# Optimization experiments

Hardware: AMD Instinct MI355X
Metric: run time of the kernel (lower is better)

Reference implementation:

```python
import jax, jax.numpy as jnp
import numpy as np

N_NODE = 100000
H = 128          # hidden_size
N_INTEREST = 4
B = 4096         # batch
T = 50           # session length


def setup_inputs() -> dict:
    key = jax.random.key(0)
    ks = jax.random.split(key, 8)
    stdv = 1.0 / np.sqrt(H)
    u = lambda k, s: jax.random.uniform(k, s, jnp.float32, -stdv, stdv)
    return {
        "inputs": jax.random.randint(ks[0], (B, T), 0, N_NODE),
        "embedding": u(ks[1], (N_NODE, H)),            # nn.Embedding weight
        "w_interest": u(ks[2], (N_INTEREST, H)),       # Linear(H -> n_interest, bias=False)
        "w_ih": u(ks[3], (N_INTEREST, 3 * H, H)),      # per-interest GNN params
        "w_hh": u(ks[4], (N_INTEREST, 3 * H, H)),
        "b_ih": u(ks[5], (N_INTEREST, 3 * H)),
        "b_hh": u(ks[6], (N_INTEREST, 3 * H)),
        "h0": jax.random.normal(ks[7], (N_INTEREST, B, H), jnp.float32),  # torch.randn init state
    }


def _gru_interest(w_ih, w_hh, b_ih, b_hh, h0, g_t, x_t):
    """Custom gated recurrence for one interest. x_t: [T,B,H], g_t: [T,B]."""
    def step(h, inp):
        x, gv = inp
        gi = x @ w_ih.T + b_ih          # [B, 3H]
        gh = h @ w_hh.T + b_hh          # [B, 3H]
        i_r, i_i, i_n = jnp.split(gi, 3, axis=1)
        h_r, h_i, h_n = jnp.split(gh, 3, axis=1)
        resetgate = jax.nn.sigmoid(i_r + h_r)
        inputgate = jax.nn.sigmoid(i_i + h_i)
        newgate = jnp.tanh(i_n + resetgate * h_n)
        g = gv[:, None]                  # [B, 1]
        concentrgate = jnp.where(g > 0.01, 1.0, 0.0) * g * inputgate
        hy = (1.0 - concentrgate) * h + concentrgate * newgate
        return hy, None
    h_last, _ = jax.lax.scan(step, h0, (x_t, g_t))
    return h_last                        # [B, H]


def reference(inputs, embedding, w_interest, w_ih, w_hh, b_ih, b_hh, h0):
    hidden = embedding[inputs]                                   # [B, T, H]
    # item_weight_for_interest: softmax over interests with temperature 0.1
    g = jax.nn.softmax((hidden @ w_interest.T) / 0.1, axis=2)    # [B, T, I]
    x_t = jnp.transpose(hidden, (1, 0, 2))                       # [T, B, H]
    g_t = jnp.transpose(g, (2, 1, 0))                            # [I, T, B]
    out = jax.vmap(_gru_interest, in_axes=(0, 0, 0, 0, 0, 0, None))(
        w_ih, w_hh, b_ih, b_hh, h0, g_t, x_t)                    # [I, B, H]
    return jnp.transpose(out, (1, 0, 2))                         # [B, I, H]
```

## Files before the change

kernel.cpp:

```cpp
#include <hip/hip_runtime.h>
#include <hip/hip_bf16.h>

#define NB 4096
#define NT 50
#define NH 128
#define NINT 4
#define ROWS 64

typedef float f32x4 __attribute__((ext_vector_type(4)));
typedef __bf16 bf16x8 __attribute__((ext_vector_type(8)));
typedef short short8 __attribute__((ext_vector_type(8)));
typedef short short4s __attribute__((ext_vector_type(4)));

#define L2E 1.4426950408889634f

__device__ __forceinline__ float frcp(float x) { return __builtin_amdgcn_rcpf(x); }

__device__ __forceinline__ float exp2neg(float x) {
  float r;
  asm("v_exp_f32 %0, -%1" : "=v"(r) : "v"(x));
  return r;
}

__device__ __forceinline__ unsigned short bfbits(float f) {
  __bf16 b = (__bf16)f;
  return __builtin_bit_cast(unsigned short, b);
}

__global__ __launch_bounds__(512, 2)
void gru_fused(const int* __restrict__ inputs, const float* __restrict__ emb,
               const float* __restrict__ w_int, const float* __restrict__ w_ih,
               const float* __restrict__ w_hh, const float* __restrict__ b_ih,
               const float* __restrict__ b_hh, const float* __restrict__ h0,
               float* __restrict__ out) {
  __shared__ unsigned short xs[2][ROWS * NH];
  __shared__ unsigned short hs[2][ROWS * NH];
  __shared__ int idxs[NT * ROWS];

  const int tid = threadIdx.x;
  const int bx = blockIdx.x;
  const int I = bx >> 6;
  const int R0 = (bx & 63) * ROWS;
  const int w = tid >> 6;
  const int lane = tid & 63;
  const int l15 = lane & 15;
  const int l4 = lane >> 4;
  const int oc0 = w * 16 + l4 * 4;

  const int sr = tid >> 3;
  const int sp = tid & 7;

  for (int e = tid; e < NT * ROWS; e += 512) {
    int t = e >> 6, r = e & (ROWS - 1);
    idxs[e] = inputs[(size_t)(R0 + r) * NT + t];
  }
  __syncthreads();

  bf16x8 wih[3][4], whh[3][4];
  f32x4 bR, bI, bNI, bNH;
  {
    const float gs[3] = {L2E, L2E, 2.0f * L2E};
    #pragma unroll
    for (int g = 0; g < 3; ++g) {
      int oc = g * NH + w * 16 + l15;
      #pragma unroll
      for (int kk = 0; kk < 4; ++kk) {
        int k0 = kk * 32 + l4 * 8;
        const float* pi = w_ih + ((size_t)(I * 384 + oc) * NH + k0);
        const float* ph = w_hh + ((size_t)(I * 384 + oc) * NH + k0);
        bf16x8 si, sh;
        #pragma unroll
        for (int e = 0; e < 8; ++e) {
          si[e] = (__bf16)(pi[e] * gs[g]);
          sh[e] = (__bf16)(ph[e] * gs[g]);
        }
        wih[g][kk] = si;
        whh[g][kk] = sh;
      }
    }
    #pragma unroll
    for (int j = 0; j < 4; ++j) {
      bR[j] = (b_ih[I * 384 + oc0 + j] + b_hh[I * 384 + oc0 + j]) * L2E;
      bI[j] = (b_ih[I * 384 + NH + oc0 + j] + b_hh[I * 384 + NH + oc0 + j]) * L2E;
      bNI[j] = b_ih[I * 384 + 2 * NH + oc0 + j] * (2.0f * L2E);
      bNH[j] = b_hh[I * 384 + 2 * NH + oc0 + j] * (2.0f * L2E);
    }
  }

  bf16x8 wg[4];
  #pragma unroll
  for (int kk = 0; kk < 4; ++kk) {
    bf16x8 f;
    #pragma unroll
    for (int e = 0; e < 8; ++e) {
      float v = (l15 < NINT)
                    ? w_int[l15 * NH + kk * 32 + l4 * 8 + e] * (10.0f * L2E)
                    : 0.0f;
      f[e] = (__bf16)v;
    }
    wg[kk] = f;
  }

  float hm[4][4];
  #pragma unroll
  for (int m = 0; m < 4; ++m) {
    int row = m * 16 + l15;
    short4s p;
    #pragma unroll
    for (int j = 0; j < 4; ++j) {
      float v = h0[((size_t)I * NB + R0 + row) * NH + oc0 + j];
      hm[m][j] = v;
      p[j] = (short)bfbits(v);
    }
    *(short4s*)&hs[0][(row * NH + oc0) ^ ((row & 7) << 3)] = p;
  }

  {
    const float4* src = (const float4*)(emb + (size_t)idxs[sr] * NH + sp * 16);
    float4 v0 = src[0], v1 = src[1], v2 = src[2], v3 = src[3];
    short8 s0, s1;
    s0[0] = bfbits(v0.x); s0[1] = bfbits(v0.y); s0[2] = bfbits(v0.z); s0[3] = bfbits(v0.w);
    s0[4] = bfbits(v1.x); s0[5] = bfbits(v1.y); s0[6] = bfbits(v1.z); s0[7] = bfbits(v1.w);
    s1[0] = bfbits(v2.x); s1[1] = bfbits(v2.y); s1[2] = bfbits(v2.z); s1[3] = bfbits(v2.w);
    s1[4] = bfbits(v3.x); s1[5] = bfbits(v3.y); s1[6] = bfbits(v3.z); s1[7] = bfbits(v3.w);
    int base = sr * NH + sp * 16;
    int sw = (sr & 7) << 3;
    *(short8*)&xs[0][base ^ sw] = s0;
    *(short8*)&xs[0][(base + 8) ^ sw] = s1;
  }
  __syncthreads();

  for (int t = 0; t < NT; ++t) {
    const int cur = t & 1, nxt = cur ^ 1;
    const bool pf = (t + 1 < NT);

    float4 v0, v1, v2, v3;
    if (pf) {
      const float4* src =
          (const float4*)(emb + (size_t)idxs[(t + 1) * ROWS + sr] * NH + sp * 16);
      v0 = src[0]; v1 = src[1]; v2 = src[2]; v3 = src[3];
    }

    const unsigned short* hsc = hs[cur];
    const unsigned short* xsc = xs[cur];
    unsigned short* hsn = hs[nxt];

    #pragma unroll
    for (int m = 0; m < 4; ++m) {
      f32x4 aR = bR, aI = bI, aNI = bNI, aNH = bNH;
      f32x4 aG = f32x4{0.0f, 0.0f, 0.0f, 0.0f};

      int brow = m * 16 + l15;
      int blin = brow * NH + l4 * 8;
      int sw2 = (brow & 7) << 3;
      __builtin_amdgcn_s_setprio(1);
      #pragma unroll
      for (int kk = 0; kk < 4; ++kk) {
        int e = (blin + kk * 32) ^ sw2;
        bf16x8 bh = __builtin_bit_cast(bf16x8, *(const short8*)&hsc[e]);
        bf16x8 bx = __builtin_bit_cast(bf16x8, *(const short8*)&xsc[e]);
        aG = __builtin_amdgcn_mfma_f32_16x16x32_bf16(wg[kk], bx, aG, 0, 0, 0);
        aR = __builtin_amdgcn_mfma_f32_16x16x32_bf16(wih[0][kk], bx, aR, 0, 0, 0);
        aR = __builtin_amdgcn_mfma_f32_16x16x32_bf16(whh[0][kk], bh, aR, 0, 0, 0);
        aI = __builtin_amdgcn_mfma_f32_16x16x32_bf16(wih[1][kk], bx, aI, 0, 0, 0);
        aI = __builtin_amdgcn_mfma_f32_16x16x32_bf16(whh[1][kk], bh, aI, 0, 0, 0);
        aNI = __builtin_amdgcn_mfma_f32_16x16x32_bf16(wih[2][kk], bx, aNI, 0, 0, 0);
        aNH = __builtin_amdgcn_mfma_f32_16x16x32_bf16(whh[2][kk], bh, aNH, 0, 0, 0);
      }
      __builtin_amdgcn_s_setprio(0);

      float s0 = aG[0], s1 = aG[1], s2 = aG[2], s3 = aG[3];
      float mx = fmaxf(fmaxf(s0, s1), fmaxf(s2, s3));
      float e0 = exp2neg(mx - s0), e1 = exp2neg(mx - s1);
      float e2 = exp2neg(mx - s2), e3 = exp2neg(mx - s3);
      float sel = (I == 0) ? e0 : (I == 1) ? e1 : (I == 2) ? e2 : e3;
      float gvl = sel * frcp(e0 + e1 + e2 + e3);
      gvl = (gvl > 0.01f) ? gvl : 0.0f;
      const float gv = __shfl(gvl, l15, 64);

      short4s p;
      #pragma unroll
      for (int j = 0; j < 4; ++j) {
        float rg = frcp(1.0f + exp2neg(aR[j]));
        float ig = frcp(1.0f + exp2neg(aI[j]));
        float an = fmaf(rg, aNH[j], aNI[j]);
        float ng = fmaf(2.0f, frcp(1.0f + exp2neg(an)), -1.0f);
        float c = gv * ig;
        float hy = fmaf(c, ng - hm[m][j], hm[m][j]);
        hm[m][j] = hy;
        p[j] = (short)bfbits(hy);
      }
      *(short4s*)&hsn[(brow * NH + oc0) ^ sw2] = p;
    }

    if (pf) {
      short8 s0, s1;
      s0[0] = bfbits(v0.x); s0[1] = bfbits(v0.y); s0[2] = bfbits(v0.z); s0[3] = bfbits(v0.w);
      s0[4] = bfbits(v1.x); s0[5] = bfbits(v1.y); s0[6] = bfbits(v1.z); s0[7] = bfbits(v1.w);
      s1[0] = bfbits(v2.x); s1[1] = bfbits(v2.y); s1[2] = bfbits(v2.z); s1[3] = bfbits(v2.w);
      s1[4] = bfbits(v3.x); s1[5] = bfbits(v3.y); s1[6] = bfbits(v3.z); s1[7] = bfbits(v3.w);
      int base = sr * NH + sp * 16;
      int sw = (sr & 7) << 3;
      *(short8*)&xs[nxt][base ^ sw] = s0;
      *(short8*)&xs[nxt][(base + 8) ^ sw] = s1;
    }
    __syncthreads();
  }

  #pragma unroll
  for (int m = 0; m < 4; ++m) {
    int row = m * 16 + l15;
    f32x4 o;
    #pragma unroll
    for (int j = 0; j < 4; ++j) o[j] = hm[m][j];
    *(f32x4*)&out[(size_t)(R0 + row) * (NINT * NH) + I * NH + oc0] = o;
  }
}

extern "C" void kernel_launch(void* const* d_in, const int* in_sizes, int n_in,
                              void* d_out, int out_size, void* d_ws, size_t ws_size,
                              hipStream_t stream) {
  const int* inputs = (const int*)d_in[0];
  const float* emb = (const float*)d_in[1];
  const float* w_int = (const float*)d_in[2];
  const float* w_ih = (const float*)d_in[3];
  const float* w_hh = (const float*)d_in[4];
  const float* b_ih = (const float*)d_in[5];
  const float* b_hh = (const float*)d_in[6];
  const float* h0 = (const float*)d_in[7];
  float* out = (float*)d_out;

  dim3 grid(NINT * (NB / ROWS));
  dim3 block(512);
  gru_fused<<<grid, block, 0, stream>>>(inputs, emb, w_int, w_ih, w_hh, b_ih,
                                        b_hh, h0, out);
}
```

Before: 193.0 us.

## Batch two row tiles per MFMA phase and stagger tile order across waves

Each step now groups the four 16-row tiles into pairs: the MFMAs for both tiles of a pair run back to back before their gate math. Half of the waves (chosen by a parity over the wave index) process the pairs in reverse order, so MFMA phases of some waves line up with the transcendental gate phases of others on the same SIMD. The softmax max-subtraction is also dropped, which relies on the bounded logits not overflowing exp2. Holding two tiles' accumulators at once raises register pressure under the 512x2 launch bounds and could cause spills.

```diff
diff --git a/kernel.cpp b/kernel.cpp
--- a/kernel.cpp
+++ b/kernel.cpp
@@ -46,6 +46,7 @@
   const int l15 = lane & 15;
   const int l4 = lane >> 4;
   const int oc0 = w * 16 + l4 * 4;
+  const int po = (w + (w >> 2)) & 1;
 
   const int sr = tid >> 3;
   const int sp = tid & 7;
@@ -130,6 +131,60 @@
   }
   __syncthreads();
 
+#define GRU_PAIR(MP)                                                           \
+  {                                                                            \
+    f32x4 aG[2], aR[2], aI[2], aNI[2], aNH[2];                                 \
+    __builtin_amdgcn_s_setprio(1);                                             \
+    _Pragma("unroll")                                                          \
+    for (int m2 = 0; m2 < 2; ++m2) {                                           \
+      const int m = (MP)*2 + m2;                                               \
+      aG[m2] = f32x4{0.0f, 0.0f, 0.0f, 0.0f};                                  \
+      aR[m2] = bR; aI[m2] = bI; aNI[m2] = bNI; aNH[m2] = bNH;                  \
+      int brow = m * 16 + l15;                                                 \
+      int blin = brow * NH + l4 * 8;                                           \
+      int sw2 = (brow & 7) << 3;                                               \
+      _Pragma("unroll")                                                        \
+      for (int kk = 0; kk < 4; ++kk) {                                         \
+        int e = (blin + kk * 32) ^ sw2;                                        \
+        bf16x8 bh = __builtin_bit_cast(bf16x8, *(const short8*)&hsc[e]);       \
+        bf16x8 bx = __builtin_bit_cast(bf16x8, *(const short8*)&xsc[e]);       \
+        aG[m2] = __builtin_amdgcn_mfma_f32_16x16x32_bf16(wg[kk], bx, aG[m2], 0, 0, 0);      \
+        aR[m2] = __builtin_amdgcn_mfma_f32_16x16x32_bf16(wih[0][kk], bx, aR[m2], 0, 0, 0);  \
+        aR[m2] = __builtin_amdgcn_mfma_f32_16x16x32_bf16(whh[0][kk], bh, aR[m2], 0, 0, 0);  \
+        aI[m2] = __builtin_amdgcn_mfma_f32_16x16x32_bf16(wih[1][kk], bx, aI[m2], 0, 0, 0);  \
+        aI[m2] = __builtin_amdgcn_mfma_f32_16x16x32_bf16(whh[1][kk], bh, aI[m2], 0, 0, 0);  \
+        aNI[m2] = __builtin_amdgcn_mfma_f32_16x16x32_bf16(wih[2][kk], bx, aNI[m2], 0, 0, 0);\
+        aNH[m2] = __builtin_amdgcn_mfma_f32_16x16x32_bf16(whh[2][kk], bh, aNH[m2], 0, 0, 0);\
+      }                                                                        \
+    }                                                                          \
+    __builtin_amdgcn_s_setprio(0);                                             \
+    _Pragma("unroll")                                                          \
+    for (int m2 = 0; m2 < 2; ++m2) {                                           \
+      const int m = (MP)*2 + m2;                                               \
+      int brow = m * 16 + l15;                                                 \
+      int sw2 = (brow & 7) << 3;                                               \
+      float e0 = exp2neg(-aG[m2][0]), e1 = exp2neg(-aG[m2][1]);                \
+      float e2 = exp2neg(-aG[m2][2]), e3 = exp2neg(-aG[m2][3]);                \
+      float sel = (I == 0) ? e0 : (I == 1) ? e1 : (I == 2) ? e2 : e3;          \
+      float gvl = sel * frcp(e0 + e1 + e2 + e3);                               \
+      gvl = (gvl > 0.01f) ? gvl : 0.0f;                                        \
+      const float gv = __shfl(gvl, l15, 64);                                   \
+      short4s p;                                                               \
+      _Pragma("unroll")                                                        \
+      for (int j = 0; j < 4; ++j) {                                            \
+        float rg = frcp(1.0f + exp2neg(aR[m2][j]));                            \
+        float ig = frcp(1.0f + exp2neg(aI[m2][j]));                            \
+        float an = fmaf(rg, aNH[m2][j], aNI[m2][j]);                           \
+        float ng = fmaf(2.0f, frcp(1.0f + exp2neg(an)), -1.0f);                \
+        float c = gv * ig;                                                     \
+        float hy = fmaf(c, ng - hm[m][j], hm[m][j]);                           \
+        hm[m][j] = hy;                                                         \
+        p[j] = (short)bfbits(hy);                                              \
+      }                                                                        \
+      *(short4s*)&hsn[(brow * NH + oc0) ^ sw2] = p;                            \
+    }                                                                          \
+  }
+
   for (int t = 0; t < NT; ++t) {
     const int cur = t & 1, nxt = cur ^ 1;
     const bool pf = (t + 1 < NT);
@@ -145,52 +200,12 @@
     const unsigned short* xsc = xs[cur];
     unsigned short* hsn = hs[nxt];
 
-    #pragma unroll
-    for (int m = 0; m < 4; ++m) {
-      f32x4 aR = bR, aI = bI, aNI = bNI, aNH = bNH;
-      f32x4 aG = f32x4{0.0f, 0.0f, 0.0f, 0.0f};
-
-      int brow = m * 16 + l15;
-      int blin = brow * NH + l4 * 8;
-      int sw2 = (brow & 7) << 3;
-      __builtin_amdgcn_s_setprio(1);
-      #pragma unroll
-      for (int kk = 0; kk < 4; ++kk) {
-        int e = (blin + kk * 32) ^ sw2;
-        bf16x8 bh = __builtin_bit_cast(bf16x8, *(const short8*)&hsc[e]);
-        bf16x8 bx = __builtin_bit_cast(bf16x8, *(const short8*)&xsc[e]);
-        aG = __builtin_amdgcn_mfma_f32_16x16x32_bf16(wg[kk], bx, aG, 0, 0, 0);
-        aR = __builtin_amdgcn_mfma_f32_16x16x32_bf16(wih[0][kk], bx, aR, 0, 0, 0);
-        aR = __builtin_amdgcn_mfma_f32_16x16x32_bf16(whh[0][kk], bh, aR, 0, 0, 0);
-        aI = __builtin_amdgcn_mfma_f32_16x16x32_bf16(wih[1][kk], bx, aI, 0, 0, 0);
-        aI = __builtin_amdgcn_mfma_f32_16x16x32_bf16(whh[1][kk], bh, aI, 0, 0, 0);
-        aNI = __builtin_amdgcn_mfma_f32_16x16x32_bf16(wih[2][kk], bx, aNI, 0, 0, 0);
-        aNH = __builtin_amdgcn_mfma_f32_16x16x32_bf16(whh[2][kk], bh, aNH, 0, 0, 0);
-      }
-      __builtin_amdgcn_s_setprio(0);
-
-      float s0 = aG[0], s1 = aG[1], s2 = aG[2], s3 = aG[3];
-      float mx = fmaxf(fmaxf(s0, s1), fmaxf(s2, s3));
-      float e0 = exp2neg(mx - s0), e1 = exp2neg(mx - s1);
-      float e2 = exp2neg(mx - s2), e3 = exp2neg(mx - s3);
-      float sel = (I == 0) ? e0 : (I == 1) ? e1 : (I == 2) ? e2 : e3;
-      float gvl = sel * frcp(e0 + e1 + e2 + e3);
-      gvl = (gvl > 0.01f) ? gvl : 0.0f;
-      const float gv = __shfl(gvl, l15, 64);
-
-      short4s p;
-      #pragma unroll
-      for (int j = 0; j < 4; ++j) {
-        float rg = frcp(1.0f + exp2neg(aR[j]));
-        float ig = frcp(1.0f + exp2neg(aI[j]));
-        float an = fmaf(rg, aNH[j], aNI[j]);
-        float ng = fmaf(2.0f, frcp(1.0f + exp2neg(an)), -1.0f);
-        float c = gv * ig;
-        float hy = fmaf(c, ng - hm[m][j], hm[m][j]);
-        hm[m][j] = hy;
-        p[j] = (short)bfbits(hy);
-      }
-      *(short4s*)&hsn[(brow * NH + oc0) ^ sw2] = p;
+    if (po == 0) {
+      GRU_PAIR(0);
+      GRU_PAIR(1);
+    } else {
+      GRU_PAIR(1);
+      GRU_PAIR(0);
     }
 
     if (pf) {
```

Result: slower. 258.4 us (+33.9%).
